# Kernel tuning notes

Measured on AMD Instinct MI355X. Metric: run time of the kernel, lower is better.

## Reference

```python
import jax, jax.numpy as jnp
import numpy as np

N = 100000      # nodes
E = 1600000     # edges (before self loops)
G = 64          # graphs (drones)
H = 4           # heads
C = 64          # hidden_channels (per-head dim, concat=False)
NODE_F = 32
DRONE_F = 16
OUT = 32
L = 2           # num_layers
LN_EPS = 1e-5
NEG_SLOPE = 0.2


def setup_inputs() -> dict:
    key = jax.random.key(0)
    ks = jax.random.split(key, 20)
    gn = lambda k, shape, s=0.1: jax.random.normal(k, shape, jnp.float32) * s
    inp = {}
    inp["x"] = jax.random.normal(ks[0], (N, NODE_F), jnp.float32)
    inp["drone_feat"] = jax.random.normal(ks[1], (G, DRONE_F), jnp.float32)
    inp["edge_index"] = jax.random.randint(ks[2], (2, E), 0, N, jnp.int32)
    inp["batch"] = jnp.sort(jax.random.randint(ks[3], (N,), 0, G, jnp.int32))
    inp["node_W"] = gn(ks[4], (C, NODE_F)); inp["node_b"] = jnp.zeros((C,), jnp.float32)
    inp["drone_W"] = gn(ks[5], (C, DRONE_F)); inp["drone_b"] = jnp.zeros((C,), jnp.float32)
    for l in range(L):
        kk = jax.random.split(ks[6 + l], 3)
        inp[f"convW{l}"] = gn(kk[0], (H * C, C))
        inp[f"att_src{l}"] = gn(kk[1], (H, C))
        inp[f"att_dst{l}"] = gn(kk[2], (H, C))
        inp[f"convb{l}"] = jnp.zeros((C,), jnp.float32)
        inp[f"ln_g{l}"] = jnp.ones((C,), jnp.float32)
        inp[f"ln_b{l}"] = jnp.zeros((C,), jnp.float32)
    inp["out_W"] = gn(ks[10], (OUT, C)); inp["out_b"] = jnp.zeros((OUT,), jnp.float32)
    return inp


def _layer_norm(x, g, b):
    mu = jnp.mean(x, axis=-1, keepdims=True)
    var = jnp.mean((x - mu) ** 2, axis=-1, keepdims=True)
    return (x - mu) * jax.lax.rsqrt(var + LN_EPS) * g + b


def _gat_conv(h, src, dst, W, a_src, a_dst, b):
    # h: [N, C] -> per-head transform [N, H, C]
    xh = (h @ W.T).reshape(N, H, C)
    alpha_s = jnp.sum(xh * a_src[None], axis=-1)  # [N, H]
    alpha_d = jnp.sum(xh * a_dst[None], axis=-1)  # [N, H]
    e = jax.nn.leaky_relu(alpha_s[src] + alpha_d[dst], NEG_SLOPE)  # [E', H]
    m = jax.ops.segment_max(e, dst, num_segments=N)  # segment softmax over dst
    ex = jnp.exp(e - m[dst])
    s = jax.ops.segment_sum(ex, dst, num_segments=N)
    alpha = ex / (s[dst] + 1e-16)                   # [E', H]
    out = jax.ops.segment_sum(xh[src] * alpha[:, :, None], dst, num_segments=N)
    return jnp.mean(out, axis=1) + b                # concat=False -> head mean


def reference(x, edge_index, drone_feat, batch, node_W, node_b, drone_W, drone_b,
              convW0, att_src0, att_dst0, convb0, ln_g0, ln_b0,
              convW1, att_src1, att_dst1, convb1, ln_g1, ln_b1,
              out_W, out_b):
    # add self loops (PyG GATConv default add_self_loops=True)
    loop = jnp.arange(N, dtype=edge_index.dtype)
    src = jnp.concatenate([edge_index[0], loop])
    dst = jnp.concatenate([edge_index[1], loop])
    h = x @ node_W.T + node_b + (drone_feat @ drone_W.T + drone_b)[batch]
    layers = [(convW0, att_src0, att_dst0, convb0, ln_g0, ln_b0),
              (convW1, att_src1, att_dst1, convb1, ln_g1, ln_b1)]
    for (W, a_s, a_d, cb, g, lb) in layers:
        h = h + jax.nn.relu(_layer_norm(_gat_conv(h, src, dst, W, a_s, a_d, cb), g, lb))
    return h @ out_W.T + out_b
```

## Files before the change

kernel.cpp:

```cpp
#include <hip/hip_runtime.h>
#include <hip/hip_bf16.h>
#include <hip/hip_fp16.h>
#include <math.h>


#define NEG_SLOPE 0.2f
#define LN_EPS 1e-5f

struct __align__(8) h16x4 { __half x, y, z, w; };

__global__ __launch_bounds__(256) void k_h0(
        const float* __restrict__ x, const int* __restrict__ batch,
        const float* __restrict__ node_W, const float* __restrict__ drone_W,
        const float* __restrict__ node_b, const float* __restrict__ drone_b,
        const float* __restrict__ drone_feat,
        float* __restrict__ h, int* __restrict__ cnt, int* __restrict__ csrB, int N) {
    __shared__ float xs[16][33];
    __shared__ float ds[16][17];
    __shared__ float wn[32][65];
    __shared__ float wd[16][65];
    __shared__ float bs[64];
    int t = threadIdx.x;
    int n0 = blockIdx.x * 16;
    for (int i = t; i < 2048; i += 256) { int co = i >> 5, k = i & 31; wn[k][co] = node_W[i]; }
    for (int i = t; i < 1024; i += 256) { int co = i >> 4, k = i & 15; wd[k][co] = drone_W[i]; }
    if (t < 64) bs[t] = node_b[t] + drone_b[t];
    for (int i = t; i < 512; i += 256) {
        int r = i >> 5, c = i & 31;
        int n = n0 + r;
        xs[r][c] = (n < N) ? x[(size_t)n * 32 + c] : 0.f;
    }
    {
        int r = t >> 4, c = t & 15;
        int n = n0 + r;
        int g = (n < N) ? batch[n] : 0;
        ds[r][c] = drone_feat[g * 16 + c];
    }
    {
        int gt = blockIdx.x * 256 + t;
        if (gt < N) { cnt[gt] = 1; csrB[(size_t)gt << 6] = gt; }
    }
    __syncthreads();
    int co = t & 63;
    int nsub = t >> 6;
    float b = bs[co];
    float a0 = b, a1 = b, a2 = b, a3 = b;
#pragma unroll
    for (int k = 0; k < 32; ++k) {
        float w = wn[k][co];
        a0 = fmaf(xs[nsub * 4 + 0][k], w, a0);
        a1 = fmaf(xs[nsub * 4 + 1][k], w, a1);
        a2 = fmaf(xs[nsub * 4 + 2][k], w, a2);
        a3 = fmaf(xs[nsub * 4 + 3][k], w, a3);
    }
#pragma unroll
    for (int k = 0; k < 16; ++k) {
        float w = wd[k][co];
        a0 = fmaf(ds[nsub * 4 + 0][k], w, a0);
        a1 = fmaf(ds[nsub * 4 + 1][k], w, a1);
        a2 = fmaf(ds[nsub * 4 + 2][k], w, a2);
        a3 = fmaf(ds[nsub * 4 + 3][k], w, a3);
    }
    float av[4] = {a0, a1, a2, a3};
#pragma unroll
    for (int j = 0; j < 4; ++j) {
        int n = n0 + nsub * 4 + j;
        if (n < N) h[(size_t)n * 64 + co] = av[j];
    }
}

__global__ void k_scatter(const int* __restrict__ edge_index, int* __restrict__ cnt,
                          int* __restrict__ csrB,
                          const float* __restrict__ cW0, const float* __restrict__ cW1,
                          const float* __restrict__ s0, const float* __restrict__ d0,
                          const float* __restrict__ s1, const float* __restrict__ d1,
                          const float* __restrict__ out_W,
                          float* __restrict__ wt0, float* __restrict__ wt1,
                          float* __restrict__ uv, float* __restrict__ owT,
                          int E, int S) {
    if (blockIdx.y == 0 && blockIdx.x < 128) {
        int i = blockIdx.x * 256 + threadIdx.x;
        {
            int j = i & 16383;
            int co = j >> 6, k = j & 63;
            if (i < 16384) wt0[k * 256 + co] = cW0[j];
            else           wt1[k * 256 + co] = cW1[j];
        }
        if (i < 2048) {
            int k = i >> 5, o = i & 31;
            owT[i] = out_W[o * 64 + k];
        }
        if (i < 1024) {
            int l = i >> 9, sd = (i >> 8) & 1, head = (i >> 6) & 3, kk = i & 63;
            const float* W   = l ? cW1 : cW0;
            const float* att = l ? (sd ? d1 : s1) : (sd ? d0 : s0);
            float acc = 0.f;
            for (int c = 0; c < 64; ++c)
                acc += W[(head * 64 + c) * 64 + kk] * att[head * 64 + c];
            uv[i] = acc;
        }
    }
    int lo = blockIdx.y * S, hi = lo + S;
    int i = (blockIdx.x * blockDim.x + threadIdx.x) * 4;
    if (i + 3 < E) {
        int4 sv = *(const int4*)(edge_index + i);
        int4 dv = *(const int4*)(edge_index + E + i);
        if (dv.x >= lo && dv.x < hi) { int sl = atomicAdd(cnt + dv.x, 1); if (sl < 64) csrB[((size_t)dv.x << 6) + sl] = sv.x; }
        if (dv.y >= lo && dv.y < hi) { int sl = atomicAdd(cnt + dv.y, 1); if (sl < 64) csrB[((size_t)dv.y << 6) + sl] = sv.y; }
        if (dv.z >= lo && dv.z < hi) { int sl = atomicAdd(cnt + dv.z, 1); if (sl < 64) csrB[((size_t)dv.z << 6) + sl] = sv.z; }
        if (dv.w >= lo && dv.w < hi) { int sl = atomicAdd(cnt + dv.w, 1); if (sl < 64) csrB[((size_t)dv.w << 6) + sl] = sv.w; }
    } else {
        for (int k = i; k < E; ++k) {
            int d = edge_index[E + k];
            if (d >= lo && d < hi) { int sl = atomicAdd(cnt + d, 1); if (sl < 64) csrB[((size_t)d << 6) + sl] = edge_index[k]; }
        }
    }
}

#define XPAD 68
__global__ __launch_bounds__(256) void k_xh(
        const float* __restrict__ h, const float* __restrict__ wt,
        const float* __restrict__ uv_l, __half* __restrict__ xh,
        float* __restrict__ as_, float* __restrict__ ad_, int N) {
    __shared__ float hs[32][XPAD];
    int t = threadIdx.x;
    int n0 = blockIdx.x * 32;
    for (int i = t; i < 32 * 64; i += 256) {
        int r = i >> 6, c = i & 63;
        int n = n0 + r;
        hs[r][c] = (n < N) ? h[(size_t)n * 64 + c] : 0.f;
    }
    __syncthreads();
    int co4 = (t & 63) * 4;
    int nsub = t >> 6;
    float4 acc[8];
#pragma unroll
    for (int j = 0; j < 8; ++j) acc[j] = make_float4(0.f, 0.f, 0.f, 0.f);
    const float* wp = wt + co4;
#pragma unroll 2
    for (int k4 = 0; k4 < 16; ++k4) {
        float4 w0 = *(const float4*)(wp + (k4 * 4 + 0) * 256);
        float4 w1 = *(const float4*)(wp + (k4 * 4 + 1) * 256);
        float4 w2 = *(const float4*)(wp + (k4 * 4 + 2) * 256);
        float4 w3 = *(const float4*)(wp + (k4 * 4 + 3) * 256);
#pragma unroll
        for (int j = 0; j < 8; ++j) {
            float4 hv = *(const float4*)&hs[nsub * 8 + j][k4 * 4];
            float4 a = acc[j];
            a.x = fmaf(hv.x, w0.x, fmaf(hv.y, w1.x, fmaf(hv.z, w2.x, fmaf(hv.w, w3.x, a.x))));
            a.y = fmaf(hv.x, w0.y, fmaf(hv.y, w1.y, fmaf(hv.z, w2.y, fmaf(hv.w, w3.y, a.y))));
            a.z = fmaf(hv.x, w0.z, fmaf(hv.y, w1.z, fmaf(hv.z, w2.z, fmaf(hv.w, w3.z, a.z))));
            a.w = fmaf(hv.x, w0.w, fmaf(hv.y, w1.w, fmaf(hv.z, w2.w, fmaf(hv.w, w3.w, a.w))));
            acc[j] = a;
        }
    }
#pragma unroll
    for (int j = 0; j < 8; ++j) {
        int n = n0 + nsub * 8 + j;
        if (n < N) {
            h16x4 o;
            o.x = __float2half(acc[j].x);
            o.y = __float2half(acc[j].y);
            o.z = __float2half(acc[j].z);
            o.w = __float2half(acc[j].w);
            *(h16x4*)(xh + (size_t)n * 256 + co4) = o;
        }
    }
    {
        int row  = t >> 3;
        int head = (t >> 1) & 3;
        int sd   = t & 1;
        int n = n0 + row;
        if (n < N) {
            const float* u = uv_l + sd * 256 + head * 64;
            float a = 0.f;
#pragma unroll
            for (int k4 = 0; k4 < 16; ++k4) {
                float4 hv = *(const float4*)&hs[row][k4 * 4];
                float4 uu = *(const float4*)(u + k4 * 4);
                a += hv.x * uu.x + hv.y * uu.y + hv.z * uu.z + hv.w * uu.w;
            }
            (sd ? ad_ : as_)[n * 4 + head] = a;
        }
    }
}

__device__ inline __half2 shxor_h2(__half2 a, int m) {
    int u = __shfl_xor(*(int*)&a, m, 64);
    return *(__half2*)&u;
}

template <bool LAST>
__global__ __launch_bounds__(256) void k_gat(
        const __half* __restrict__ xh, const float* __restrict__ as_,
        const float* __restrict__ ad_, const int* __restrict__ cnt,
        const int* __restrict__ csrB, const float* __restrict__ convb,
        const float* __restrict__ ln_g, const float* __restrict__ ln_b,
        float* __restrict__ h, const float* __restrict__ owT,
        const float* __restrict__ out_b, float* __restrict__ out, int N) {
    int wid = threadIdx.x >> 6, lane = threadIdx.x & 63;
    int n = blockIdx.x * 4 + wid;
    if (n >= N) return;
    int g    = lane >> 4;
    int l16  = lane & 15;
    int head = l16 >> 2;
    int r0 = n << 6;
    int r1 = r0 + min(cnt[n], 64);
    float adv = ad_[(size_t)n * 4 + head];
    const __half* xb = xh + (size_t)l16 * 16;

    float s = 0.f;
    __half2 acc[8];
#pragma unroll
    for (int j = 0; j < 8; ++j) acc[j] = __float2half2_rn(0.f);

    uint4 zero4 = make_uint4(0u, 0u, 0u, 0u);
    int idx;
    idx = r0 + g;        bool vA = idx < r1; int sA = 0; if (vA) sA = csrB[idx];
    idx = r0 + 4 + g;    bool vB = idx < r1; int sB = 0; if (vB) sB = csrB[idx];
    idx = r0 + 8 + g;    bool vC = idx < r1; int sC = 0; if (vC) sC = csrB[idx];
    idx = r0 + 12 + g;   bool vD = idx < r1; int sD = 0; if (vD) sD = csrB[idx];
    float asA = 0.f, asB = 0.f;
    uint4 qA0 = zero4, qA1 = zero4, qB0 = zero4, qB1 = zero4;
    if (vA) {
        asA = as_[(size_t)sA * 4 + head];
        const uint4* bp = (const uint4*)(xb + (size_t)sA * 256);
        qA0 = bp[0]; qA1 = bp[1];
    }
    if (vB) {
        asB = as_[(size_t)sB * 4 + head];
        const uint4* bp = (const uint4*)(xb + (size_t)sB * 256);
        qB0 = bp[0]; qB1 = bp[1];
    }

    auto COMPUTE = [&](bool vc, float asc, const uint4& q0, const uint4& q1) {
        float e = asc + adv;
        e = e > 0.f ? e : NEG_SLOPE * e;
        float w = __expf(e);
        w = vc ? w : 0.f;
        s += w;
        __half2 w2 = __float2half2_rn(w);
        const __half2* ha = (const __half2*)&q0;
        const __half2* hb = (const __half2*)&q1;
        acc[0] = __hfma2(w2, ha[0], acc[0]);
        acc[1] = __hfma2(w2, ha[1], acc[1]);
        acc[2] = __hfma2(w2, ha[2], acc[2]);
        acc[3] = __hfma2(w2, ha[3], acc[3]);
        acc[4] = __hfma2(w2, hb[0], acc[4]);
        acc[5] = __hfma2(w2, hb[1], acc[5]);
        acc[6] = __hfma2(w2, hb[2], acc[6]);
        acc[7] = __hfma2(w2, hb[3], acc[7]);
    };

    for (int i = r0; i < r1; i += 8) {
        COMPUTE(vA, asA, qA0, qA1);
        int idxE = i + 16 + g; bool vE = idxE < r1; int sE = 0;
        if (vE) sE = csrB[idxE];
        vA = vC;
        if (vC) {
            asA = as_[(size_t)sC * 4 + head];
            const uint4* bp = (const uint4*)(xb + (size_t)sC * 256);
            qA0 = bp[0]; qA1 = bp[1];
        }
        COMPUTE(vB, asB, qB0, qB1);
        int idxF = i + 20 + g; bool vF = idxF < r1; int sF = 0;
        if (vF) sF = csrB[idxF];
        vB = vD;
        if (vD) {
            asB = as_[(size_t)sD * 4 + head];
            const uint4* bp = (const uint4*)(xb + (size_t)sD * 256);
            qB0 = bp[0]; qB1 = bp[1];
        }
        vC = vE; sC = sE;
        vD = vF; sD = sF;
    }

    s += __shfl_xor(s, 16, 64);
    s += __shfl_xor(s, 32, 64);
#pragma unroll
    for (int j = 0; j < 8; ++j) {
        acc[j] = __hadd2(acc[j], shxor_h2(acc[j], 16));
        acc[j] = __hadd2(acc[j], shxor_h2(acc[j], 32));
    }
    float inv = 1.f / (s + 1e-16f);
    float f[16];
#pragma unroll
    for (int j = 0; j < 8; ++j) {
        float2 tv = __half22float2(acc[j]);
        f[2 * j]     = tv.x * inv;
        f[2 * j + 1] = tv.y * inv;
    }
#pragma unroll
    for (int j = 0; j < 16; ++j) {
        f[j] += __shfl_xor(f[j], 4, 64);
        f[j] += __shfl_xor(f[j], 8, 64);
    }
    int cblk = lane & 3;
    int cb16 = cblk * 16;
    float o[16];
    float part = 0.f;
#pragma unroll
    for (int q = 0; q < 4; ++q) {
        float4 cb = *(const float4*)(convb + cb16 + q * 4);
        o[q * 4 + 0] = 0.25f * f[q * 4 + 0] + cb.x;
        o[q * 4 + 1] = 0.25f * f[q * 4 + 1] + cb.y;
        o[q * 4 + 2] = 0.25f * f[q * 4 + 2] + cb.z;
        o[q * 4 + 3] = 0.25f * f[q * 4 + 3] + cb.w;
        part += o[q * 4 + 0] + o[q * 4 + 1] + o[q * 4 + 2] + o[q * 4 + 3];
    }
    part += __shfl_xor(part, 1, 64);
    part += __shfl_xor(part, 2, 64);
    float mu = part * (1.f / 64.f);
    float vs = 0.f;
#pragma unroll
    for (int j = 0; j < 16; ++j) { o[j] -= mu; vs += o[j] * o[j]; }
    vs += __shfl_xor(vs, 1, 64);
    vs += __shfl_xor(vs, 2, 64);
    float rstd = rsqrtf(vs * (1.f / 64.f) + LN_EPS);

    float hout[16];
    {
        const float4* hp = (const float4*)(h + (size_t)n * 64 + cb16);
        const float4* gp = (const float4*)(ln_g + cb16);
        const float4* bp = (const float4*)(ln_b + cb16);
#pragma unroll
        for (int q = 0; q < 4; ++q) {
            float4 hv = hp[q];
            float4 gv = gp[q];
            float4 bv = bp[q];
            hout[q * 4 + 0] = hv.x + fmaxf(o[q * 4 + 0] * rstd * gv.x + bv.x, 0.f);
            hout[q * 4 + 1] = hv.y + fmaxf(o[q * 4 + 1] * rstd * gv.y + bv.y, 0.f);
            hout[q * 4 + 2] = hv.z + fmaxf(o[q * 4 + 2] * rstd * gv.z + bv.z, 0.f);
            hout[q * 4 + 3] = hv.w + fmaxf(o[q * 4 + 3] * rstd * gv.w + bv.w, 0.f);
        }
    }
    if (!LAST) {
        if (lane < 4) {
            float4* hw = (float4*)(h + (size_t)n * 64 + cb16);
#pragma unroll
            for (int q = 0; q < 4; ++q)
                hw[q] = make_float4(hout[q * 4 + 0], hout[q * 4 + 1],
                                    hout[q * 4 + 2], hout[q * 4 + 3]);
        }
    } else {
        int oc = lane & 31;
        float acc2 = out_b[oc];
#pragma unroll
        for (int l4 = 0; l4 < 4; ++l4) {
#pragma unroll
            for (int j = 0; j < 16; ++j) {
                float hv = __shfl(hout[j], l4, 64);
                acc2 = fmaf(hv, owT[(l4 * 16 + j) * 32 + oc], acc2);
            }
        }
        if (lane < 32) out[(size_t)n * 32 + oc] = acc2;
    }
}

static inline unsigned cdiv(long long a, long long b) { return (unsigned)((a + b - 1) / b); }

extern "C" void kernel_launch(void* const* d_in, const int* in_sizes, int n_in,
                              void* d_out, int out_size, void* d_ws, size_t ws_size,
                              hipStream_t stream) {
    const float* x          = (const float*)d_in[0];
    const float* drone_feat = (const float*)d_in[1];
    const int*   edge_index = (const int*)d_in[2];
    const int*   batch      = (const int*)d_in[3];
    const float* node_W     = (const float*)d_in[4];
    const float* node_b     = (const float*)d_in[5];
    const float* drone_W    = (const float*)d_in[6];
    const float* drone_b    = (const float*)d_in[7];
    const float* convW[2]   = {(const float*)d_in[8],  (const float*)d_in[14]};
    const float* att_src[2] = {(const float*)d_in[9],  (const float*)d_in[15]};
    const float* att_dst[2] = {(const float*)d_in[10], (const float*)d_in[16]};
    const float* convb[2]   = {(const float*)d_in[11], (const float*)d_in[17]};
    const float* ln_g[2]    = {(const float*)d_in[12], (const float*)d_in[18]};
    const float* ln_b[2]    = {(const float*)d_in[13], (const float*)d_in[19]};
    const float* out_W      = (const float*)d_in[20];
    const float* out_b      = (const float*)d_in[21];
    float* out = (float*)d_out;

    const int N = in_sizes[0] / 32;
    const int E = in_sizes[2] / 2;
    const int P = 8;
    const int S = cdiv(N, P);

    char* base = (char*)d_ws;
    size_t off = 0;
    auto alloc = [&](size_t bytes) {
        char* p = base + off;
        off = (off + bytes + 255) & ~(size_t)255;
        return p;
    };
    float*           h      = (float*)alloc((size_t)N * 64 * 4);
    __half*          xh     = (__half*)alloc((size_t)N * 256 * 2);
    float*           as_    = (float*)alloc((size_t)N * 4 * 4);
    float*           ad_    = (float*)alloc((size_t)N * 4 * 4);
    float*           wt0    = (float*)alloc((size_t)256 * 64 * 4);
    float*           wt1    = (float*)alloc((size_t)256 * 64 * 4);
    float*           uv     = (float*)alloc((size_t)1024 * 4);
    float*           owT    = (float*)alloc((size_t)2048 * 4);
    int*             cnt    = (int*)alloc((size_t)N * 4);
    int*             csrB   = (int*)alloc((size_t)N * 64 * 4);
    (void)ws_size;
    const float* wt[2] = {wt0, wt1};

    k_h0<<<cdiv(N, 16), 256, 0, stream>>>(x, batch, node_W, drone_W, node_b, drone_b,
                                          drone_feat, h, cnt, csrB, N);
    {
        dim3 g(cdiv(cdiv(E, 4), 256), P);
        k_scatter<<<g, 256, 0, stream>>>(edge_index, cnt, csrB,
                                         convW[0], convW[1], att_src[0], att_dst[0],
                                         att_src[1], att_dst[1], out_W,
                                         wt0, wt1, uv, owT, E, S);
    }
    k_xh<<<cdiv(N, 32), 256, 0, stream>>>(h, wt[0], uv + 0 * 512, xh, as_, ad_, N);
    k_gat<false><<<cdiv(N, 4), 256, 0, stream>>>(xh, as_, ad_, cnt, csrB, convb[0],
                                                 ln_g[0], ln_b[0], h, owT, out_b, out, N);
    k_xh<<<cdiv(N, 32), 256, 0, stream>>>(h, wt[1], uv + 1 * 512, xh, as_, ad_, N);
    k_gat<true><<<cdiv(N, 4), 256, 0, stream>>>(xh, as_, ad_, cnt, csrB, convb[1],
                                                ln_g[1], ln_b[1], h, owT, out_b, out, N);
}
```

Measured before the change: 698.1 us.

## Fuse all phases into one persistent kernel with software grid barriers

Replaces the six separate launches (h0, scatter, two xh, two gat) with a single persistent kernel sized to occupancy. Phases are separated by atomic-counter grid barriers, and work is distributed with grid-stride loops. The 8-partition edge scatter now runs as sequential passes inside the persistent grid. The final output projection now goes through LDS instead of shuffles. This removes launch gaps and tail effects, but adds barrier spin cost and depends on all blocks being co-resident, with a spin-count escape if they are not.

```diff
diff --git a/kernel.cpp b/kernel.cpp
--- a/kernel.cpp
+++ b/kernel.cpp
@@ -1,5 +1,4 @@
 #include <hip/hip_runtime.h>
-#include <hip/hip_bf16.h>
 #include <hip/hip_fp16.h>
 #include <math.h>
 
@@ -9,352 +8,401 @@
 
 struct __align__(8) h16x4 { __half x, y, z, w; };
 
-__global__ __launch_bounds__(256) void k_h0(
-        const float* __restrict__ x, const int* __restrict__ batch,
-        const float* __restrict__ node_W, const float* __restrict__ drone_W,
-        const float* __restrict__ node_b, const float* __restrict__ drone_b,
-        const float* __restrict__ drone_feat,
-        float* __restrict__ h, int* __restrict__ cnt, int* __restrict__ csrB, int N) {
-    __shared__ float xs[16][33];
-    __shared__ float ds[16][17];
-    __shared__ float wn[32][65];
-    __shared__ float wd[16][65];
-    __shared__ float bs[64];
-    int t = threadIdx.x;
-    int n0 = blockIdx.x * 16;
-    for (int i = t; i < 2048; i += 256) { int co = i >> 5, k = i & 31; wn[k][co] = node_W[i]; }
-    for (int i = t; i < 1024; i += 256) { int co = i >> 4, k = i & 15; wd[k][co] = drone_W[i]; }
-    if (t < 64) bs[t] = node_b[t] + drone_b[t];
-    for (int i = t; i < 512; i += 256) {
-        int r = i >> 5, c = i & 31;
-        int n = n0 + r;
-        xs[r][c] = (n < N) ? x[(size_t)n * 32 + c] : 0.f;
-    }
-    {
-        int r = t >> 4, c = t & 15;
-        int n = n0 + r;
-        int g = (n < N) ? batch[n] : 0;
-        ds[r][c] = drone_feat[g * 16 + c];
-    }
-    {
-        int gt = blockIdx.x * 256 + t;
-        if (gt < N) { cnt[gt] = 1; csrB[(size_t)gt << 6] = gt; }
-    }
+struct Params {
+    const float* x; const float* drone_feat; const int* edge_index; const int* batch;
+    const float* node_W; const float* node_b; const float* drone_W; const float* drone_b;
+    const float* cW0; const float* s0; const float* d0; const float* cb0; const float* g0; const float* lb0;
+    const float* cW1; const float* s1; const float* d1; const float* cb1; const float* g1; const float* lb1;
+    const float* out_W; const float* out_b;
+    float* out;
+    float* h; __half* xh; float* as_; float* ad_;
+    float* wt0; float* wt1; float* uv; float* owT;
+    int* cnt; int* csrB; int* bar;
+    int N; int E;
+};
+
+__device__ __forceinline__ __half2 shxor_h2(__half2 a, int m) {
+    int u = __shfl_xor(*(int*)&a, m, 64);
+    return *(__half2*)&u;
+}
+
+__device__ __forceinline__ void gbar(int* bar, int nb) {
     __syncthreads();
-    int co = t & 63;
+    if (threadIdx.x == 0) {
+        __threadfence();
+        __hip_atomic_fetch_add(bar, 1, __ATOMIC_RELEASE, __HIP_MEMORY_SCOPE_AGENT);
+        int spins = 0;
+        while (__hip_atomic_load(bar, __ATOMIC_ACQUIRE, __HIP_MEMORY_SCOPE_AGENT) < nb) {
+            __builtin_amdgcn_s_sleep(2);
+            if (++spins > (1 << 24)) break;
+        }
+        __threadfence();
+    }
+    __syncthreads();
+}
+
+__device__ __forceinline__ void xh_phase(const Params& p, const float* __restrict__ wt,
+                                         const float* __restrict__ uv_l, float* smem) {
+    const int t = threadIdx.x, bid = blockIdx.x, nb = gridDim.x;
+    const int N = p.N;
+    float* hs = smem;
+    int co4 = (t & 63) * 4;
     int nsub = t >> 6;
-    float b = bs[co];
-    float a0 = b, a1 = b, a2 = b, a3 = b;
-#pragma unroll
-    for (int k = 0; k < 32; ++k) {
-        float w = wn[k][co];
-        a0 = fmaf(xs[nsub * 4 + 0][k], w, a0);
-        a1 = fmaf(xs[nsub * 4 + 1][k], w, a1);
-        a2 = fmaf(xs[nsub * 4 + 2][k], w, a2);
-        a3 = fmaf(xs[nsub * 4 + 3][k], w, a3);
-    }
-#pragma unroll
-    for (int k = 0; k < 16; ++k) {
-        float w = wd[k][co];
-        a0 = fmaf(ds[nsub * 4 + 0][k], w, a0);
-        a1 = fmaf(ds[nsub * 4 + 1][k], w, a1);
-        a2 = fmaf(ds[nsub * 4 + 2][k], w, a2);
-        a3 = fmaf(ds[nsub * 4 + 3][k], w, a3);
-    }
-    float av[4] = {a0, a1, a2, a3};
-#pragma unroll
-    for (int j = 0; j < 4; ++j) {
-        int n = n0 + nsub * 4 + j;
-        if (n < N) h[(size_t)n * 64 + co] = av[j];
-    }
-}
-
-__global__ void k_scatter(const int* __restrict__ edge_index, int* __restrict__ cnt,
-                          int* __restrict__ csrB,
-                          const float* __restrict__ cW0, const float* __restrict__ cW1,
-                          const float* __restrict__ s0, const float* __restrict__ d0,
-                          const float* __restrict__ s1, const float* __restrict__ d1,
-                          const float* __restrict__ out_W,
-                          float* __restrict__ wt0, float* __restrict__ wt1,
-                          float* __restrict__ uv, float* __restrict__ owT,
-                          int E, int S) {
-    if (blockIdx.y == 0 && blockIdx.x < 128) {
-        int i = blockIdx.x * 256 + threadIdx.x;
+    int ntiles = (N + 31) >> 5;
+    for (int tile = bid; tile < ntiles; tile += nb) {
+        int n0 = tile << 5;
+        __syncthreads();
+        for (int i = t; i < 2048; i += 256) {
+            int r = i >> 6, c = i & 63;
+            int n = n0 + r;
+            hs[r * 68 + c] = (n < N) ? p.h[(size_t)n * 64 + c] : 0.f;
+        }
+        __syncthreads();
+        float4 acc[8];
+#pragma unroll
+        for (int j = 0; j < 8; ++j) acc[j] = make_float4(0.f, 0.f, 0.f, 0.f);
+        const float* wp = wt + co4;
+#pragma unroll 2
+        for (int k4 = 0; k4 < 16; ++k4) {
+            float4 w0 = *(const float4*)(wp + (k4 * 4 + 0) * 256);
+            float4 w1 = *(const float4*)(wp + (k4 * 4 + 1) * 256);
+            float4 w2 = *(const float4*)(wp + (k4 * 4 + 2) * 256);
+            float4 w3 = *(const float4*)(wp + (k4 * 4 + 3) * 256);
+#pragma unroll
+            for (int j = 0; j < 8; ++j) {
+                float4 hv = *(const float4*)&hs[(nsub * 8 + j) * 68 + k4 * 4];
+                float4 a = acc[j];
+                a.x = fmaf(hv.x, w0.x, fmaf(hv.y, w1.x, fmaf(hv.z, w2.x, fmaf(hv.w, w3.x, a.x))));
+                a.y = fmaf(hv.x, w0.y, fmaf(hv.y, w1.y, fmaf(hv.z, w2.y, fmaf(hv.w, w3.y, a.y))));
+                a.z = fmaf(hv.x, w0.z, fmaf(hv.y, w1.z, fmaf(hv.z, w2.z, fmaf(hv.w, w3.z, a.z))));
+                a.w = fmaf(hv.x, w0.w, fmaf(hv.y, w1.w, fmaf(hv.z, w2.w, fmaf(hv.w, w3.w, a.w))));
+                acc[j] = a;
+            }
+        }
+#pragma unroll
+        for (int j = 0; j < 8; ++j) {
+            int n = n0 + nsub * 8 + j;
+            if (n < N) {
+                h16x4 o;
+                o.x = __float2half(acc[j].x);
+                o.y = __float2half(acc[j].y);
+                o.z = __float2half(acc[j].z);
+                o.w = __float2half(acc[j].w);
+                *(h16x4*)(p.xh + (size_t)n * 256 + co4) = o;
+            }
+        }
+        {
+            int row = t >> 3;
+            int head = (t >> 1) & 3;
+            int sd = t & 1;
+            int n = n0 + row;
+            if (n < N) {
+                const float* u = uv_l + sd * 256 + head * 64;
+                float a = 0.f;
+#pragma unroll
+                for (int k4 = 0; k4 < 16; ++k4) {
+                    float4 hv = *(const float4*)&hs[row * 68 + k4 * 4];
+                    float4 uu = *(const float4*)(u + k4 * 4);
+                    a += hv.x * uu.x + hv.y * uu.y + hv.z * uu.z + hv.w * uu.w;
+                }
+                (sd ? p.ad_ : p.as_)[n * 4 + head] = a;
+            }
+        }
+    }
+}
+
+__device__ __forceinline__ void gat_phase(const Params& p, const float* __restrict__ convb,
+                                          const float* __restrict__ ln_g,
+                                          const float* __restrict__ ln_b,
+                                          bool last, float* smem) {
+    const int t = threadIdx.x, bid = blockIdx.x, nb = gridDim.x;
+    const int N = p.N;
+    int wid = t >> 6, lane = t & 63;
+    float* owT_lds = smem;
+    float* hout_lds = smem + 2048 + wid * 64;
+    if (last) {
+        for (int i = t; i < 2048; i += 256) owT_lds[i] = p.owT[i];
+        __syncthreads();
+    }
+    int g = lane >> 4;
+    int l16 = lane & 15;
+    int head = l16 >> 2;
+    const __half* xb = p.xh + (size_t)l16 * 16;
+
+    for (int base = bid * 4; base < N; base += nb * 4) {
+        int n = base + wid;
+        if (n >= N) continue;
+        int r0 = n << 6;
+        int r1 = r0 + min(p.cnt[n], 64);
+        float adv = p.ad_[(size_t)n * 4 + head];
+
+        float s = 0.f;
+        __half2 acc[8];
+#pragma unroll
+        for (int j = 0; j < 8; ++j) acc[j] = __float2half2_rn(0.f);
+
+        uint4 zero4 = make_uint4(0u, 0u, 0u, 0u);
+        int idx;
+        idx = r0 + g;      bool vA = idx < r1; int sA = 0; if (vA) sA = p.csrB[idx];
+        idx = r0 + 4 + g;  bool vB = idx < r1; int sB = 0; if (vB) sB = p.csrB[idx];
+        idx = r0 + 8 + g;  bool vC = idx < r1; int sC = 0; if (vC) sC = p.csrB[idx];
+        idx = r0 + 12 + g; bool vD = idx < r1; int sD = 0; if (vD) sD = p.csrB[idx];
+        float asA = 0.f, asB = 0.f;
+        uint4 qA0 = zero4, qA1 = zero4, qB0 = zero4, qB1 = zero4;
+        if (vA) {
+            asA = p.as_[(size_t)sA * 4 + head];
+            const uint4* bp = (const uint4*)(xb + (size_t)sA * 256);
+            qA0 = bp[0]; qA1 = bp[1];
+        }
+        if (vB) {
+            asB = p.as_[(size_t)sB * 4 + head];
+            const uint4* bp = (const uint4*)(xb + (size_t)sB * 256);
+            qB0 = bp[0]; qB1 = bp[1];
+        }
+
+        auto COMPUTE = [&](bool vc, float asc, const uint4& q0, const uint4& q1) {
+            float e = asc + adv;
+            e = e > 0.f ? e : NEG_SLOPE * e;
+            float w = __expf(e);
+            w = vc ? w : 0.f;
+            s += w;
+            __half2 w2 = __float2half2_rn(w);
+            const __half2* ha = (const __half2*)&q0;
+            const __half2* hb = (const __half2*)&q1;
+            acc[0] = __hfma2(w2, ha[0], acc[0]);
+            acc[1] = __hfma2(w2, ha[1], acc[1]);
+            acc[2] = __hfma2(w2, ha[2], acc[2]);
+            acc[3] = __hfma2(w2, ha[3], acc[3]);
+            acc[4] = __hfma2(w2, hb[0], acc[4]);
+            acc[5] = __hfma2(w2, hb[1], acc[5]);
+            acc[6] = __hfma2(w2, hb[2], acc[6]);
+            acc[7] = __hfma2(w2, hb[3], acc[7]);
+        };
+
+        for (int i = r0; i < r1; i += 8) {
+            COMPUTE(vA, asA, qA0, qA1);
+            int idxE = i + 16 + g; bool vE = idxE < r1; int sE = 0;
+            if (vE) sE = p.csrB[idxE];
+            vA = vC;
+            if (vC) {
+                asA = p.as_[(size_t)sC * 4 + head];
+                const uint4* bp = (const uint4*)(xb + (size_t)sC * 256);
+                qA0 = bp[0]; qA1 = bp[1];
+            }
+            COMPUTE(vB, asB, qB0, qB1);
+            int idxF = i + 20 + g; bool vF = idxF < r1; int sF = 0;
+            if (vF) sF = p.csrB[idxF];
+            vB = vD;
+            if (vD) {
+                asB = p.as_[(size_t)sD * 4 + head];
+                const uint4* bp = (const uint4*)(xb + (size_t)sD * 256);
+                qB0 = bp[0]; qB1 = bp[1];
+            }
+            vC = vE; sC = sE;
+            vD = vF; sD = sF;
+        }
+
+        s += __shfl_xor(s, 16, 64);
+        s += __shfl_xor(s, 32, 64);
+#pragma unroll
+        for (int j = 0; j < 8; ++j) {
+            acc[j] = __hadd2(acc[j], shxor_h2(acc[j], 16));
+            acc[j] = __hadd2(acc[j], shxor_h2(acc[j], 32));
+        }
+        float inv = 1.f / (s + 1e-16f);
+        float f[16];
+#pragma unroll
+        for (int j = 0; j < 8; ++j) {
+            float2 tv = __half22float2(acc[j]);
+            f[2 * j] = tv.x * inv;
+            f[2 * j + 1] = tv.y * inv;
+        }
+#pragma unroll
+        for (int j = 0; j < 16; ++j) {
+            f[j] += __shfl_xor(f[j], 4, 64);
+            f[j] += __shfl_xor(f[j], 8, 64);
+        }
+        int cblk = lane & 3;
+        int cb16 = cblk * 16;
+        float o[16];
+        float part = 0.f;
+#pragma unroll
+        for (int q = 0; q < 4; ++q) {
+            float4 cb = *(const float4*)(convb + cb16 + q * 4);
+            o[q * 4 + 0] = 0.25f * f[q * 4 + 0] + cb.x;
+            o[q * 4 + 1] = 0.25f * f[q * 4 + 1] + cb.y;
+            o[q * 4 + 2] = 0.25f * f[q * 4 + 2] + cb.z;
+            o[q * 4 + 3] = 0.25f * f[q * 4 + 3] + cb.w;
+            part += o[q * 4 + 0] + o[q * 4 + 1] + o[q * 4 + 2] + o[q * 4 + 3];
+        }
+        part += __shfl_xor(part, 1, 64);
+        part += __shfl_xor(part, 2, 64);
+        float mu = part * (1.f / 64.f);
+        float vs = 0.f;
+#pragma unroll
+        for (int j = 0; j < 16; ++j) { o[j] -= mu; vs += o[j] * o[j]; }
+        vs += __shfl_xor(vs, 1, 64);
+        vs += __shfl_xor(vs, 2, 64);
+        float rstd = rsqrtf(vs * (1.f / 64.f) + LN_EPS);
+
+        if (!last) {
+            if (lane < 4) {
+                float4* hp = (float4*)(p.h + (size_t)n * 64 + cb16);
+#pragma unroll
+                for (int q = 0; q < 4; ++q) {
+                    float4 hv = hp[q];
+                    float4 gv = *(const float4*)(ln_g + cb16 + q * 4);
+                    float4 bv = *(const float4*)(ln_b + cb16 + q * 4);
+                    hv.x += fmaxf(o[q * 4 + 0] * rstd * gv.x + bv.x, 0.f);
+                    hv.y += fmaxf(o[q * 4 + 1] * rstd * gv.y + bv.y, 0.f);
+                    hv.z += fmaxf(o[q * 4 + 2] * rstd * gv.z + bv.z, 0.f);
+                    hv.w += fmaxf(o[q * 4 + 3] * rstd * gv.w + bv.w, 0.f);
+                    hp[q] = hv;
+                }
+            }
+        } else {
+            if (lane < 4) {
+                const float4* hp = (const float4*)(p.h + (size_t)n * 64 + cb16);
+#pragma unroll
+                for (int q = 0; q < 4; ++q) {
+                    float4 hv = hp[q];
+                    float4 gv = *(const float4*)(ln_g + cb16 + q * 4);
+                    float4 bv = *(const float4*)(ln_b + cb16 + q * 4);
+                    hout_lds[cb16 + q * 4 + 0] = hv.x + fmaxf(o[q * 4 + 0] * rstd * gv.x + bv.x, 0.f);
+                    hout_lds[cb16 + q * 4 + 1] = hv.y + fmaxf(o[q * 4 + 1] * rstd * gv.y + bv.y, 0.f);
+                    hout_lds[cb16 + q * 4 + 2] = hv.z + fmaxf(o[q * 4 + 2] * rstd * gv.z + bv.z, 0.f);
+                    hout_lds[cb16 + q * 4 + 3] = hv.w + fmaxf(o[q * 4 + 3] * rstd * gv.w + bv.w, 0.f);
+                }
+            }
+            asm volatile("s_waitcnt lgkmcnt(0)" ::: "memory");
+            if (lane < 32) {
+                float acc2 = p.out_b[lane];
+#pragma unroll 8
+                for (int k = 0; k < 64; ++k)
+                    acc2 = fmaf(hout_lds[k], owT_lds[k * 32 + lane], acc2);
+                p.out[(size_t)n * 32 + lane] = acc2;
+            }
+        }
+    }
+}
+
+__global__ __launch_bounds__(256) void k_fused(Params p) {
+    __shared__ float smem[4096];
+    const int t = threadIdx.x;
+    const int bid = blockIdx.x;
+    const int nb = gridDim.x;
+    const int N = p.N, E = p.E;
+
+    if (bid < 128) {
+        int i = bid * 256 + t;
         {
             int j = i & 16383;
             int co = j >> 6, k = j & 63;
-            if (i < 16384) wt0[k * 256 + co] = cW0[j];
-            else           wt1[k * 256 + co] = cW1[j];
-        }
-        if (i < 2048) {
-            int k = i >> 5, o = i & 31;
-            owT[i] = out_W[o * 64 + k];
-        }
+            if (i < 16384) p.wt0[k * 256 + co] = p.cW0[j];
+            else           p.wt1[k * 256 + co] = p.cW1[j];
+        }
+        if (i < 2048) { int k = i >> 5, o = i & 31; p.owT[i] = p.out_W[o * 64 + k]; }
         if (i < 1024) {
             int l = i >> 9, sd = (i >> 8) & 1, head = (i >> 6) & 3, kk = i & 63;
-            const float* W   = l ? cW1 : cW0;
-            const float* att = l ? (sd ? d1 : s1) : (sd ? d0 : s0);
+            const float* W   = l ? p.cW1 : p.cW0;
+            const float* att = l ? (sd ? p.d1 : p.s1) : (sd ? p.d0 : p.s0);
             float acc = 0.f;
             for (int c = 0; c < 64; ++c)
                 acc += W[(head * 64 + c) * 64 + kk] * att[head * 64 + c];
-            uv[i] = acc;
-        }
-    }
-    int lo = blockIdx.y * S, hi = lo + S;
-    int i = (blockIdx.x * blockDim.x + threadIdx.x) * 4;
-    if (i + 3 < E) {
-        int4 sv = *(const int4*)(edge_index + i);
-        int4 dv = *(const int4*)(edge_index + E + i);
-        if (dv.x >= lo && dv.x < hi) { int sl = atomicAdd(cnt + dv.x, 1); if (sl < 64) csrB[((size_t)dv.x << 6) + sl] = sv.x; }
-        if (dv.y >= lo && dv.y < hi) { int sl = atomicAdd(cnt + dv.y, 1); if (sl < 64) csrB[((size_t)dv.y << 6) + sl] = sv.y; }
-        if (dv.z >= lo && dv.z < hi) { int sl = atomicAdd(cnt + dv.z, 1); if (sl < 64) csrB[((size_t)dv.z << 6) + sl] = sv.z; }
-        if (dv.w >= lo && dv.w < hi) { int sl = atomicAdd(cnt + dv.w, 1); if (sl < 64) csrB[((size_t)dv.w << 6) + sl] = sv.w; }
-    } else {
-        for (int k = i; k < E; ++k) {
-            int d = edge_index[E + k];
-            if (d >= lo && d < hi) { int sl = atomicAdd(cnt + d, 1); if (sl < 64) csrB[((size_t)d << 6) + sl] = edge_index[k]; }
-        }
-    }
-}
-
-#define XPAD 68
-__global__ __launch_bounds__(256) void k_xh(
-        const float* __restrict__ h, const float* __restrict__ wt,
-        const float* __restrict__ uv_l, __half* __restrict__ xh,
-        float* __restrict__ as_, float* __restrict__ ad_, int N) {
-    __shared__ float hs[32][XPAD];
-    int t = threadIdx.x;
-    int n0 = blockIdx.x * 32;
-    for (int i = t; i < 32 * 64; i += 256) {
-        int r = i >> 6, c = i & 63;
-        int n = n0 + r;
-        hs[r][c] = (n < N) ? h[(size_t)n * 64 + c] : 0.f;
-    }
-    __syncthreads();
-    int co4 = (t & 63) * 4;
-    int nsub = t >> 6;
-    float4 acc[8];
-#pragma unroll
-    for (int j = 0; j < 8; ++j) acc[j] = make_float4(0.f, 0.f, 0.f, 0.f);
-    const float* wp = wt + co4;
-#pragma unroll 2
-    for (int k4 = 0; k4 < 16; ++k4) {
-        float4 w0 = *(const float4*)(wp + (k4 * 4 + 0) * 256);
-        float4 w1 = *(const float4*)(wp + (k4 * 4 + 1) * 256);
-        float4 w2 = *(const float4*)(wp + (k4 * 4 + 2) * 256);
-        float4 w3 = *(const float4*)(wp + (k4 * 4 + 3) * 256);
-#pragma unroll
-        for (int j = 0; j < 8; ++j) {
-            float4 hv = *(const float4*)&hs[nsub * 8 + j][k4 * 4];
-            float4 a = acc[j];
-            a.x = fmaf(hv.x, w0.x, fmaf(hv.y, w1.x, fmaf(hv.z, w2.x, fmaf(hv.w, w3.x, a.x))));
-            a.y = fmaf(hv.x, w0.y, fmaf(hv.y, w1.y, fmaf(hv.z, w2.y, fmaf(hv.w, w3.y, a.y))));
-            a.z = fmaf(hv.x, w0.z, fmaf(hv.y, w1.z, fmaf(hv.z, w2.z, fmaf(hv.w, w3.z, a.z))));
-            a.w = fmaf(hv.x, w0.w, fmaf(hv.y, w1.w, fmaf(hv.z, w2.w, fmaf(hv.w, w3.w, a.w))));
-            acc[j] = a;
-        }
-    }
-#pragma unroll
-    for (int j = 0; j < 8; ++j) {
-        int n = n0 + nsub * 8 + j;
-        if (n < N) {
-            h16x4 o;
-            o.x = __float2half(acc[j].x);
-            o.y = __float2half(acc[j].y);
-            o.z = __float2half(acc[j].z);
-            o.w = __float2half(acc[j].w);
-            *(h16x4*)(xh + (size_t)n * 256 + co4) = o;
-        }
+            p.uv[i] = acc;
+        }
+    }
+    for (int gt = bid * 256 + t; gt < N; gt += nb * 256) {
+        p.cnt[gt] = 1;
+        p.csrB[(size_t)gt << 6] = gt;
     }
     {
-        int row  = t >> 3;
-        int head = (t >> 1) & 3;
-        int sd   = t & 1;
-        int n = n0 + row;
-        if (n < N) {
-            const float* u = uv_l + sd * 256 + head * 64;
-            float a = 0.f;
-#pragma unroll
-            for (int k4 = 0; k4 < 16; ++k4) {
-                float4 hv = *(const float4*)&hs[row][k4 * 4];
-                float4 uu = *(const float4*)(u + k4 * 4);
-                a += hv.x * uu.x + hv.y * uu.y + hv.z * uu.z + hv.w * uu.w;
-            }
-            (sd ? ad_ : as_)[n * 4 + head] = a;
-        }
-    }
-}
-
-__device__ inline __half2 shxor_h2(__half2 a, int m) {
-    int u = __shfl_xor(*(int*)&a, m, 64);
-    return *(__half2*)&u;
-}
-
-template <bool LAST>
-__global__ __launch_bounds__(256) void k_gat(
-        const __half* __restrict__ xh, const float* __restrict__ as_,
-        const float* __restrict__ ad_, const int* __restrict__ cnt,
-        const int* __restrict__ csrB, const float* __restrict__ convb,
-        const float* __restrict__ ln_g, const float* __restrict__ ln_b,
-        float* __restrict__ h, const float* __restrict__ owT,
-        const float* __restrict__ out_b, float* __restrict__ out, int N) {
-    int wid = threadIdx.x >> 6, lane = threadIdx.x & 63;
-    int n = blockIdx.x * 4 + wid;
-    if (n >= N) return;
-    int g    = lane >> 4;
-    int l16  = lane & 15;
-    int head = l16 >> 2;
-    int r0 = n << 6;
-    int r1 = r0 + min(cnt[n], 64);
-    float adv = ad_[(size_t)n * 4 + head];
-    const __half* xb = xh + (size_t)l16 * 16;
-
-    float s = 0.f;
-    __half2 acc[8];
-#pragma unroll
-    for (int j = 0; j < 8; ++j) acc[j] = __float2half2_rn(0.f);
-
-    uint4 zero4 = make_uint4(0u, 0u, 0u, 0u);
-    int idx;
-    idx = r0 + g;        bool vA = idx < r1; int sA = 0; if (vA) sA = csrB[idx];
-    idx = r0 + 4 + g;    bool vB = idx < r1; int sB = 0; if (vB) sB = csrB[idx];
-    idx = r0 + 8 + g;    bool vC = idx < r1; int sC = 0; if (vC) sC = csrB[idx];
-    idx = r0 + 12 + g;   bool vD = idx < r1; int sD = 0; if (vD) sD = csrB[idx];
-    float asA = 0.f, asB = 0.f;
-    uint4 qA0 = zero4, qA1 = zero4, qB0 = zero4, qB1 = zero4;
-    if (vA) {
-        asA = as_[(size_t)sA * 4 + head];
-        const uint4* bp = (const uint4*)(xb + (size_t)sA * 256);
-        qA0 = bp[0]; qA1 = bp[1];
-    }
-    if (vB) {
-        asB = as_[(size_t)sB * 4 + head];
-        const uint4* bp = (const uint4*)(xb + (size_t)sB * 256);
-        qB0 = bp[0]; qB1 = bp[1];
-    }
-
-    auto COMPUTE = [&](bool vc, float asc, const uint4& q0, const uint4& q1) {
-        float e = asc + adv;
-        e = e > 0.f ? e : NEG_SLOPE * e;
-        float w = __expf(e);
-        w = vc ? w : 0.f;
-        s += w;
-        __half2 w2 = __float2half2_rn(w);
-        const __half2* ha = (const __half2*)&q0;
-        const __half2* hb = (const __half2*)&q1;
-        acc[0] = __hfma2(w2, ha[0], acc[0]);
-        acc[1] = __hfma2(w2, ha[1], acc[1]);
-        acc[2] = __hfma2(w2, ha[2], acc[2]);
-        acc[3] = __hfma2(w2, ha[3], acc[3]);
-        acc[4] = __hfma2(w2, hb[0], acc[4]);
-        acc[5] = __hfma2(w2, hb[1], acc[5]);
-        acc[6] = __hfma2(w2, hb[2], acc[6]);
-        acc[7] = __hfma2(w2, hb[3], acc[7]);
-    };
-
-    for (int i = r0; i < r1; i += 8) {
-        COMPUTE(vA, asA, qA0, qA1);
-        int idxE = i + 16 + g; bool vE = idxE < r1; int sE = 0;
-        if (vE) sE = csrB[idxE];
-        vA = vC;
-        if (vC) {
-            asA = as_[(size_t)sC * 4 + head];
-            const uint4* bp = (const uint4*)(xb + (size_t)sC * 256);
-            qA0 = bp[0]; qA1 = bp[1];
-        }
-        COMPUTE(vB, asB, qB0, qB1);
-        int idxF = i + 20 + g; bool vF = idxF < r1; int sF = 0;
-        if (vF) sF = csrB[idxF];
-        vB = vD;
-        if (vD) {
-            asB = as_[(size_t)sD * 4 + head];
-            const uint4* bp = (const uint4*)(xb + (size_t)sD * 256);
-            qB0 = bp[0]; qB1 = bp[1];
-        }
-        vC = vE; sC = sE;
-        vD = vF; sD = sF;
-    }
-
-    s += __shfl_xor(s, 16, 64);
-    s += __shfl_xor(s, 32, 64);
-#pragma unroll
-    for (int j = 0; j < 8; ++j) {
-        acc[j] = __hadd2(acc[j], shxor_h2(acc[j], 16));
-        acc[j] = __hadd2(acc[j], shxor_h2(acc[j], 32));
-    }
-    float inv = 1.f / (s + 1e-16f);
-    float f[16];
-#pragma unroll
-    for (int j = 0; j < 8; ++j) {
-        float2 tv = __half22float2(acc[j]);
-        f[2 * j]     = tv.x * inv;
-        f[2 * j + 1] = tv.y * inv;
-    }
-#pragma unroll
-    for (int j = 0; j < 16; ++j) {
-        f[j] += __shfl_xor(f[j], 4, 64);
-        f[j] += __shfl_xor(f[j], 8, 64);
-    }
-    int cblk = lane & 3;
-    int cb16 = cblk * 16;
-    float o[16];
-    float part = 0.f;
-#pragma unroll
-    for (int q = 0; q < 4; ++q) {
-        float4 cb = *(const float4*)(convb + cb16 + q * 4);
-        o[q * 4 + 0] = 0.25f * f[q * 4 + 0] + cb.x;
-        o[q * 4 + 1] = 0.25f * f[q * 4 + 1] + cb.y;
-        o[q * 4 + 2] = 0.25f * f[q * 4 + 2] + cb.z;
-        o[q * 4 + 3] = 0.25f * f[q * 4 + 3] + cb.w;
-        part += o[q * 4 + 0] + o[q * 4 + 1] + o[q * 4 + 2] + o[q * 4 + 3];
-    }
-    part += __shfl_xor(part, 1, 64);
-    part += __shfl_xor(part, 2, 64);
-    float mu = part * (1.f / 64.f);
-    float vs = 0.f;
-#pragma unroll
-    for (int j = 0; j < 16; ++j) { o[j] -= mu; vs += o[j] * o[j]; }
-    vs += __shfl_xor(vs, 1, 64);
-    vs += __shfl_xor(vs, 2, 64);
-    float rstd = rsqrtf(vs * (1.f / 64.f) + LN_EPS);
-
-    float hout[16];
+        float* wn = smem;
+        float* wd = smem + 2080;
+        float* bs = smem + 3120;
+        float* xs = smem + 3184;
+        float* ds = smem + 3712;
+        for (int i = t; i < 2048; i += 256) { int co = i >> 5, k = i & 31; wn[k * 65 + co] = p.node_W[i]; }
+        for (int i = t; i < 1024; i += 256) { int co = i >> 4, k = i & 15; wd[k * 65 + co] = p.drone_W[i]; }
+        if (t < 64) bs[t] = p.node_b[t] + p.drone_b[t];
+        int co = t & 63, nsub = t >> 6;
+        int ntiles = (N + 15) >> 4;
+        for (int tile = bid; tile < ntiles; tile += nb) {
+            int n0 = tile << 4;
+            __syncthreads();
+            for (int i = t; i < 512; i += 256) {
+                int r = i >> 5, c = i & 31;
+                int n = n0 + r;
+                xs[r * 33 + c] = (n < N) ? p.x[(size_t)n * 32 + c] : 0.f;
+            }
+            {
+                int r = t >> 4, c = t & 15;
+                int n = n0 + r;
+                int g = (n < N) ? p.batch[n] : 0;
+                ds[r * 17 + c] = p.drone_feat[g * 16 + c];
+            }
+            __syncthreads();
+            float b = bs[co];
+            float a0 = b, a1 = b, a2 = b, a3 = b;
+#pragma unroll
+            for (int k = 0; k < 32; ++k) {
+                float w = wn[k * 65 + co];
+                a0 = fmaf(xs[(nsub * 4 + 0) * 33 + k], w, a0);
+                a1 = fmaf(xs[(nsub * 4 + 1) * 33 + k], w, a1);
+                a2 = fmaf(xs[(nsub * 4 + 2) * 33 + k], w, a2);
+                a3 = fmaf(xs[(nsub * 4 + 3) * 33 + k], w, a3);
+            }
+#pragma unroll
+            for (int k = 0; k < 16; ++k) {
+                float w = wd[k * 65 + co];
+                a0 = fmaf(ds[(nsub * 4 + 0) * 17 + k], w, a0);
+                a1 = fmaf(ds[(nsub * 4 + 1) * 17 + k], w, a1);
+                a2 = fmaf(ds[(nsub * 4 + 2) * 17 + k], w, a2);
+                a3 = fmaf(ds[(nsub * 4 + 3) * 17 + k], w, a3);
+            }
+            float av[4] = {a0, a1, a2, a3};
+#pragma unroll
+            for (int j = 0; j < 4; ++j) {
+                int n = n0 + nsub * 4 + j;
+                if (n < N) p.h[(size_t)n * 64 + co] = av[j];
+            }
+        }
+    }
+    gbar(p.bar + 0, nb);
+
     {
-        const float4* hp = (const float4*)(h + (size_t)n * 64 + cb16);
-        const float4* gp = (const float4*)(ln_g + cb16);
-        const float4* bp = (const float4*)(ln_b + cb16);
-#pragma unroll
-        for (int q = 0; q < 4; ++q) {
-            float4 hv = hp[q];
-            float4 gv = gp[q];
-            float4 bv = bp[q];
-            hout[q * 4 + 0] = hv.x + fmaxf(o[q * 4 + 0] * rstd * gv.x + bv.x, 0.f);
-            hout[q * 4 + 1] = hv.y + fmaxf(o[q * 4 + 1] * rstd * gv.y + bv.y, 0.f);
-            hout[q * 4 + 2] = hv.z + fmaxf(o[q * 4 + 2] * rstd * gv.z + bv.z, 0.f);
-            hout[q * 4 + 3] = hv.w + fmaxf(o[q * 4 + 3] * rstd * gv.w + bv.w, 0.f);
-        }
-    }
-    if (!LAST) {
-        if (lane < 4) {
-            float4* hw = (float4*)(h + (size_t)n * 64 + cb16);
-#pragma unroll
-            for (int q = 0; q < 4; ++q)
-                hw[q] = make_float4(hout[q * 4 + 0], hout[q * 4 + 1],
-                                    hout[q * 4 + 2], hout[q * 4 + 3]);
-        }
-    } else {
-        int oc = lane & 31;
-        float acc2 = out_b[oc];
-#pragma unroll
-        for (int l4 = 0; l4 < 4; ++l4) {
-#pragma unroll
-            for (int j = 0; j < 16; ++j) {
-                float hv = __shfl(hout[j], l4, 64);
-                acc2 = fmaf(hv, owT[(l4 * 16 + j) * 32 + oc], acc2);
-            }
-        }
-        if (lane < 32) out[(size_t)n * 32 + oc] = acc2;
-    }
+        int nq = E >> 2;
+        int S = (N + 7) >> 3;
+        for (int pass = 0; pass < 8; ++pass) {
+            int lo = pass * S, hi = lo + S;
+            for (int q = bid * 256 + t; q < nq; q += nb * 256) {
+                int i = q * 4;
+                int4 sv = *(const int4*)(p.edge_index + i);
+                int4 dv = *(const int4*)(p.edge_index + E + i);
+                int sl;
+                if (dv.x >= lo && dv.x < hi) { sl = atomicAdd(p.cnt + dv.x, 1); if (sl < 64) p.csrB[((size_t)dv.x << 6) + sl] = sv.x; }
+                if (dv.y >= lo && dv.y < hi) { sl = atomicAdd(p.cnt + dv.y, 1); if (sl < 64) p.csrB[((size_t)dv.y << 6) + sl] = sv.y; }
+                if (dv.z >= lo && dv.z < hi) { sl = atomicAdd(p.cnt + dv.z, 1); if (sl < 64) p.csrB[((size_t)dv.z << 6) + sl] = sv.z; }
+                if (dv.w >= lo && dv.w < hi) { sl = atomicAdd(p.cnt + dv.w, 1); if (sl < 64) p.csrB[((size_t)dv.w << 6) + sl] = sv.w; }
+            }
+        }
+        if (bid == 0 && t < (E & 3)) {
+            int k = (E & ~3) + t;
+            int d = p.edge_index[E + k];
+            int sl = atomicAdd(p.cnt + d, 1);
+            if (sl < 64) p.csrB[((size_t)d << 6) + sl] = p.edge_index[k];
+        }
+    }
+    gbar(p.bar + 1, nb);
+
+    xh_phase(p, p.wt0, p.uv, smem);
+    gbar(p.bar + 2, nb);
+    gat_phase(p, p.cb0, p.g0, p.lb0, false, smem);
+    gbar(p.bar + 3, nb);
+
+    xh_phase(p, p.wt1, p.uv + 512, smem);
+    gbar(p.bar + 4, nb);
+    gat_phase(p, p.cb1, p.g1, p.lb1, true, smem);
 }
 
 static inline unsigned cdiv(long long a, long long b) { return (unsigned)((a + b - 1) / b); }
@@ -362,28 +410,28 @@
 extern "C" void kernel_launch(void* const* d_in, const int* in_sizes, int n_in,
                               void* d_out, int out_size, void* d_ws, size_t ws_size,
                               hipStream_t stream) {
-    const float* x          = (const float*)d_in[0];
-    const float* drone_feat = (const float*)d_in[1];
-    const int*   edge_index = (const int*)d_in[2];
-    const int*   batch      = (const int*)d_in[3];
-    const float* node_W     = (const float*)d_in[4];
-    const float* node_b     = (const float*)d_in[5];
-    const float* drone_W    = (const float*)d_in[6];
-    const float* drone_b    = (const float*)d_in[7];
-    const float* convW[2]   = {(const float*)d_in[8],  (const float*)d_in[14]};
-    const float* att_src[2] = {(const float*)d_in[9],  (const float*)d_in[15]};
-    const float* att_dst[2] = {(const float*)d_in[10], (const float*)d_in[16]};
-    const float* convb[2]   = {(const float*)d_in[11], (const float*)d_in[17]};
-    const float* ln_g[2]    = {(const float*)d_in[12], (const float*)d_in[18]};
-    const float* ln_b[2]    = {(const float*)d_in[13], (const float*)d_in[19]};
-    const float* out_W      = (const float*)d_in[20];
-    const float* out_b      = (const float*)d_in[21];
-    float* out = (float*)d_out;
+    Params pr;
+    pr.x          = (const float*)d_in[0];
+    pr.drone_feat = (const float*)d_in[1];
+    pr.edge_index = (const int*)d_in[2];
+    pr.batch      = (const int*)d_in[3];
+    pr.node_W     = (const float*)d_in[4];
+    pr.node_b     = (const float*)d_in[5];
+    pr.drone_W    = (const float*)d_in[6];
+    pr.drone_b    = (const float*)d_in[7];
+    pr.cW0 = (const float*)d_in[8];  pr.s0 = (const float*)d_in[9];
+    pr.d0  = (const float*)d_in[10]; pr.cb0 = (const float*)d_in[11];
+    pr.g0  = (const float*)d_in[12]; pr.lb0 = (const float*)d_in[13];
+    pr.cW1 = (const float*)d_in[14]; pr.s1 = (const float*)d_in[15];
+    pr.d1  = (const float*)d_in[16]; pr.cb1 = (const float*)d_in[17];
+    pr.g1  = (const float*)d_in[18]; pr.lb1 = (const float*)d_in[19];
+    pr.out_W = (const float*)d_in[20];
+    pr.out_b = (const float*)d_in[21];
+    pr.out = (float*)d_out;
 
     const int N = in_sizes[0] / 32;
     const int E = in_sizes[2] / 2;
-    const int P = 8;
-    const int S = cdiv(N, P);
+    pr.N = N; pr.E = E;
 
     char* base = (char*)d_ws;
     size_t off = 0;
@@ -392,32 +440,33 @@
         off = (off + bytes + 255) & ~(size_t)255;
         return p;
     };
-    float*           h      = (float*)alloc((size_t)N * 64 * 4);
-    __half*          xh     = (__half*)alloc((size_t)N * 256 * 2);
-    float*           as_    = (float*)alloc((size_t)N * 4 * 4);
-    float*           ad_    = (float*)alloc((size_t)N * 4 * 4);
-    float*           wt0    = (float*)alloc((size_t)256 * 64 * 4);
-    float*           wt1    = (float*)alloc((size_t)256 * 64 * 4);
-    float*           uv     = (float*)alloc((size_t)1024 * 4);
-    float*           owT    = (float*)alloc((size_t)2048 * 4);
-    int*             cnt    = (int*)alloc((size_t)N * 4);
-    int*             csrB   = (int*)alloc((size_t)N * 64 * 4);
+    pr.h    = (float*)alloc((size_t)N * 64 * 4);
+    pr.xh   = (__half*)alloc((size_t)N * 256 * 2);
+    pr.as_  = (float*)alloc((size_t)N * 4 * 4);
+    pr.ad_  = (float*)alloc((size_t)N * 4 * 4);
+    pr.wt0  = (float*)alloc((size_t)256 * 64 * 4);
+    pr.wt1  = (float*)alloc((size_t)256 * 64 * 4);
+    pr.uv   = (float*)alloc((size_t)1024 * 4);
+    pr.owT  = (float*)alloc((size_t)2048 * 4);
+    pr.cnt  = (int*)alloc((size_t)N * 4);
+    pr.csrB = (int*)alloc((size_t)N * 64 * 4);
+    pr.bar  = (int*)alloc((size_t)16 * 4);
     (void)ws_size;
-    const float* wt[2] = {wt0, wt1};
-
-    k_h0<<<cdiv(N, 16), 256, 0, stream>>>(x, batch, node_W, drone_W, node_b, drone_b,
-                                          drone_feat, h, cnt, csrB, N);
-    {
-        dim3 g(cdiv(cdiv(E, 4), 256), P);
-        k_scatter<<<g, 256, 0, stream>>>(edge_index, cnt, csrB,
-                                         convW[0], convW[1], att_src[0], att_dst[0],
-                                         att_src[1], att_dst[1], out_W,
-                                         wt0, wt1, uv, owT, E, S);
-    }
-    k_xh<<<cdiv(N, 32), 256, 0, stream>>>(h, wt[0], uv + 0 * 512, xh, as_, ad_, N);
-    k_gat<false><<<cdiv(N, 4), 256, 0, stream>>>(xh, as_, ad_, cnt, csrB, convb[0],
-                                                 ln_g[0], ln_b[0], h, owT, out_b, out, N);
-    k_xh<<<cdiv(N, 32), 256, 0, stream>>>(h, wt[1], uv + 1 * 512, xh, as_, ad_, N);
-    k_gat<true><<<cdiv(N, 4), 256, 0, stream>>>(xh, as_, ad_, cnt, csrB, convb[1],
-                                                ln_g[1], ln_b[1], h, owT, out_b, out, N);
-}
+
+    static int g_grid = 0;
+    if (g_grid == 0) {
+        int dev = 0;
+        (void)hipGetDevice(&dev);
+        int mp = 0;
+        (void)hipDeviceGetAttribute(&mp, hipDeviceAttributeMultiprocessorCount, dev);
+        int nblk = 0;
+        (void)hipOccupancyMaxActiveBlocksPerMultiprocessor(&nblk, k_fused, 256, 0);
+        if (mp <= 0) mp = 256;
+        if (nblk <= 0) nblk = 1;
+        if (nblk > 8) nblk = 8;
+        g_grid = mp * nblk;
+    }
+
+    (void)hipMemsetAsync(pr.bar, 0, 16 * 4, stream);
+    k_fused<<<g_grid, 256, 0, stream>>>(pr);
+}
```

Result: slower. 1.478 ms (+111.7%).
